# Kernel tuning notes

Hardware: AMD Instinct MI355X
Metric: run time of the kernel (lower is better)

## Reference

```python
import jax, jax.numpy as jnp
import numpy as np

E = 768      # embed_dim
P = 16       # patch size
H = 12       # heads
Dh = E // H  # 64
L = 12       # layers
IMG = 224
C = 3
N = (IMG // P) ** 2 + 1  # 197 tokens (cls + patches)
B = 64
EPS = 1e-5


def setup_inputs() -> dict:
    key = jax.random.key(0)
    ks = jax.random.split(key, 16)
    rn = lambda k, shape, s=0.02: jax.random.normal(k, shape, jnp.float32) * s
    return {
        "x": jax.random.normal(ks[0], (B, C, IMG, IMG), jnp.float32),
        "conv_w": rn(ks[1], (E, C, P, P)),
        "conv_b": jnp.zeros((E,), jnp.float32),
        "cls_embed": rn(ks[2], (1, 1, E), 1.0) * 0.02,
        "pos_embed": rn(ks[3], (1, N, E), 1.0) * 0.02,
        "ln1_s": jnp.ones((L, E), jnp.float32),
        "ln1_b": jnp.zeros((L, E), jnp.float32),
        "qkv_w": rn(ks[4], (L, H, E, 3 * Dh)),   # per-head qkv Linear weight (in,out)
        "qkv_b": jnp.zeros((L, H, 3 * Dh), jnp.float32),
        "proj_w": rn(ks[5], (L, E, E)),
        "proj_b": jnp.zeros((L, E), jnp.float32),
        "ln2_s": jnp.ones((L, E), jnp.float32),
        "ln2_b": jnp.zeros((L, E), jnp.float32),
        "fc1_w": rn(ks[6], (L, E, 4 * E)),
        "fc1_b": jnp.zeros((L, 4 * E), jnp.float32),
        "fc2_w": rn(ks[7], (L, 4 * E, E)),
        "fc2_b": jnp.zeros((L, E), jnp.float32),
    }


def _layernorm(x, s, b):
    m = jnp.mean(x, -1, keepdims=True)
    v = jnp.mean((x - m) ** 2, -1, keepdims=True)
    return (x - m) * jax.lax.rsqrt(v + EPS) * s + b


def _vit_forward(x, conv_w, conv_b, cls_embed, pos_embed,
                 ln1_s, ln1_b, qkv_w, qkv_b, proj_w, proj_b,
                 ln2_s, ln2_b, fc1_w, fc1_b, fc2_w, fc2_b):
    # Patch embedding: Conv2d stride=patch, then b c h w -> b (h w) c
    h = jax.lax.conv_general_dilated(
        x, conv_w, (P, P), 'VALID',
        dimension_numbers=('NCHW', 'OIHW', 'NCHW')) + conv_b[None, :, None, None]
    Bx = h.shape[0]
    h = h.reshape(Bx, E, -1).transpose(0, 2, 1)  # [B, 196, E]
    h = jnp.concatenate([jnp.broadcast_to(cls_embed, (Bx, 1, E)), h], axis=1)
    h = h + pos_embed  # [B, N, E]

    def block(h, p):
        l1s, l1b, qw, qb, pw, pb, l2s, l2b, f1w, f1b, f2w, f2b = p
        y = _layernorm(h, l1s, l1b)
        # per-head qkv projection, all heads at once: [B,N,H,3*Dh]
        qkv = jnp.einsum('bne,hek->bnhk', y, qw) + qb
        # torch does x.view(B,N,emb//3,3) then unbind(-1): interleaved split
        qkv = qkv.reshape(Bx, N, H, Dh, 3)
        Q, K, V = qkv[..., 0], qkv[..., 1], qkv[..., 2]
        wei = jnp.einsum('bnhd,bmhd->bhnm', Q, K) / jnp.sqrt(jnp.float32(Dh))
        wei = jax.nn.softmax(wei, axis=-1)
        att = jnp.einsum('bhnm,bmhd->bnhd', wei, V).reshape(Bx, N, H * Dh)
        h = h + att @ pw + pb  # MSA proj_back + residual (dropout=eval identity)
        y2 = _layernorm(h, l2s, l2b)
        y2 = jax.nn.gelu(y2 @ f1w + f1b, approximate=False) @ f2w + f2b
        return h + y2, None

    h, _ = jax.lax.scan(block, h, (ln1_s, ln1_b, qkv_w, qkv_b, proj_w, proj_b,
                                   ln2_s, ln2_b, fc1_w, fc1_b, fc2_w, fc2_b))
    return h


def reference(x, conv_w, conv_b, cls_embed, pos_embed,
              ln1_s, ln1_b, qkv_w, qkv_b, proj_w, proj_b,
              ln2_s, ln2_b, fc1_w, fc1_b, fc2_w, fc2_b):
    return _vit_forward(x, conv_w, conv_b, cls_embed, pos_embed,
                        ln1_s, ln1_b, qkv_w, qkv_b, proj_w, proj_b,
                        ln2_s, ln2_b, fc1_w, fc1_b, fc2_w, fc2_b)
```

## Files before the change

kernel.cpp:

```cpp
#include <hip/hip_runtime.h>
#include <hip/hip_bf16.h>
#include <math.h>

typedef __hip_bfloat16 bf16;
typedef __bf16 bf16t;
typedef __attribute__((ext_vector_type(8))) __bf16 bf16x8;
typedef __attribute__((ext_vector_type(4))) __bf16 bf16x4;
typedef __attribute__((ext_vector_type(16))) float f32x16;

#define E_DIM 768
#define HEADS 12
#define DHEAD 64
#define LAYERS 12
#define NTOK 197
#define BATCH 64
#define EPSV 1e-5f

__global__ __launch_bounds__(256) void im2col_k(const float* __restrict__ x,
                                                float* __restrict__ P,
                                                int b0, int M) {
    int task = blockIdx.x * 256 + threadIdx.x;
    if (task >= M * 96) return;
    int m = task / 96;
    int kg = task - m * 96;
    int k0 = kg * 8;
    int c = k0 >> 8, py = (k0 >> 4) & 15, px = k0 & 15;
    int bl = m / 196, pidx = m - bl * 196;
    int ph = pidx / 14, pw = pidx - ph * 14;
    const float* src = x + ((size_t)((b0 + bl) * 3 + c) * 224 + (ph * 16 + py)) * 224
                         + pw * 16 + px;
    const float4* s4 = reinterpret_cast<const float4*>(src);
    float4* d4 = reinterpret_cast<float4*>(P + (size_t)m * 768 + k0);
    d4[0] = s4[0];
    d4[1] = s4[1];
}

__global__ void embed_cls(const float* __restrict__ cls, const float* __restrict__ pos,
                          float* __restrict__ h) {
    int b = blockIdx.x, e = threadIdx.x;
    h[(size_t)b * NTOK * 768 + e] = cls[e] + pos[e];
}

__global__ __launch_bounds__(256) void layernorm_k(
    const float* __restrict__ h, float* __restrict__ y,
    const float* __restrict__ s, const float* __restrict__ bsh) {
    int tok = blockIdx.x, t = threadIdx.x;
    const float* row = h + (size_t)tok * 768;
    float v0 = row[t], v1 = row[t + 256], v2 = row[t + 512];
    float s1 = v0 + v1 + v2;
    float s2 = v0 * v0 + v1 * v1 + v2 * v2;
#pragma unroll
    for (int off = 32; off; off >>= 1) {
        s1 += __shfl_xor(s1, off);
        s2 += __shfl_xor(s2, off);
    }
    __shared__ float r1[4], r2[4];
    int wv = t >> 6, ln = t & 63;
    if (ln == 0) { r1[wv] = s1; r2[wv] = s2; }
    __syncthreads();
    s1 = r1[0] + r1[1] + r1[2] + r1[3];
    s2 = r2[0] + r2[1] + r2[2] + r2[3];
    float mean = s1 * (1.f / 768.f);
    float var = s2 * (1.f / 768.f) - mean * mean;
    float rs = rsqrtf(var + EPSV);
    float* yr = y + (size_t)tok * 768;
    yr[t]       = (v0 - mean) * rs * s[t]       + bsh[t];
    yr[t + 256] = (v1 - mean) * rs * s[t + 256] + bsh[t + 256];
    yr[t + 512] = (v2 - mean) * rs * s[t + 512] + bsh[t + 512];
}

__device__ __forceinline__ f32x16 mfma_bf16(bf16x8 a, bf16x8 b, f32x16 c) {
    return __builtin_amdgcn_mfma_f32_32x32x16_bf16(a, b, c, 0, 0, 0);
}
__device__ __forceinline__ f32x16 zero16() {
    f32x16 z;
#pragma unroll
    for (int i = 0; i < 16; ++i) z[i] = 0.f;
    return z;
}
__device__ __forceinline__ bf16x8 zbf8() {
    bf16x8 v;
#pragma unroll
    for (int i = 0; i < 8; ++i) v[i] = (__bf16)0.f;
    return v;
}
__device__ __forceinline__ unsigned pkbf(float a, float b) {
    unsigned short ua = __builtin_bit_cast(unsigned short, (__bf16)a);
    unsigned short ub = __builtin_bit_cast(unsigned short, (__bf16)b);
    return (unsigned)ua | ((unsigned)ub << 16);
}
__device__ __forceinline__ void split8(float4 u0, float4 u1, bf16x8& hi, bf16x8& lo) {
    float f[8] = {u0.x, u0.y, u0.z, u0.w, u1.x, u1.y, u1.z, u1.w};
#pragma unroll
    for (int j = 0; j < 8; ++j) {
        __bf16 h = (__bf16)f[j];
        hi[j] = h;
        lo[j] = (__bf16)(f[j] - (float)h);
    }
}

#define PLANE 2064

template <typename AT, typename CT, int TERMS>
__global__ __launch_bounds__(256, 2) void gemm_mfma(
    const AT* __restrict__ A, int lda,
    const float* __restrict__ W, int ldw,
    const float* __restrict__ bias,
    const float* __restrict__ resid,
    CT* __restrict__ C, int ldc,
    int M, int K, int flags) {
    constexpr bool SPLIT_A = (TERMS >= 3);
    const int gelu = flags & 1, perHead = flags & 2, wTrans = flags & 4;
    const int embedOut = flags & 8, qkvOut = flags & 16;
    const int n0 = blockIdx.x * 128, m0 = blockIdx.y * 128;
    const int t = threadIdx.x;

    size_t QKT = 0;
    if (qkvOut) QKT = (size_t)(M / 197) * 12 * 197 * 64;

    __shared__ __align__(16) char smem[SPLIT_A ? 4 * 8256 : 3 * 8256];
    char* sAh = smem;
    char* sWh = smem + 8256;
    char* sWl = smem + 16512;
    char* sAl = SPLIT_A ? smem + 24768 : smem;

    const AT* aptr[2]; int aoff[2]; bool aok[2];
    const float* wptr[2]; int woff[2];
    const size_t wstep = perHead ? 192 : (size_t)ldw;
#pragma unroll
    for (int p = 0; p < 2; ++p) {
        int q = t + p * 256;
        int rn = q & 127, kg = q >> 7;
        int gm = m0 + rn;
        aok[p] = gm < M;
        aptr[p] = A + (size_t)(aok[p] ? gm : 0) * lda + kg * 8;
        aoff[p] = kg * PLANE + rn * 16;
        woff[p] = kg * PLANE + rn * 16;
        if (wTrans) {
            wptr[p] = W + (size_t)(n0 + rn) * ldw + kg * 8;
        } else if (perHead) {
            int gn = n0 + rn;
            int hh = gn / 192;
            wptr[p] = W + (size_t)hh * K * 192 + (gn - hh * 192) + (size_t)(kg * 8) * 192;
        } else {
            wptr[p] = W + (n0 + rn) + (size_t)(kg * 8) * ldw;
        }
    }

    const int lane = t & 63, wv = t >> 6;
    const int wm = wv >> 1, wn = wv & 1;
    const int lr = lane & 31, lk = lane >> 5;
    const int arow0 = (wm * 64 + lr) * 16;
    const int brow0 = (wn * 64 + lr) * 16;
    f32x16 acc00 = zero16(), acc01 = zero16(), acc10 = zero16(), acc11 = zero16();

    const int nIt = K >> 5;
    for (int it = 0; it < nIt; ++it) {
        const int k0 = it << 5;
        __syncthreads();
#pragma unroll
        for (int p = 0; p < 2; ++p) {
            if constexpr (sizeof(AT) == 4) {
                float4 u0 = make_float4(0.f, 0.f, 0.f, 0.f), u1 = u0;
                if (aok[p]) {
                    const float4* s4 = reinterpret_cast<const float4*>(aptr[p] + k0);
                    u0 = s4[0]; u1 = s4[1];
                }
                bf16x8 hi, lo;
                split8(u0, u1, hi, lo);
                *reinterpret_cast<bf16x8*>(sAh + aoff[p]) = hi;
                if constexpr (SPLIT_A) *reinterpret_cast<bf16x8*>(sAl + aoff[p]) = lo;
            } else {
                bf16x8 hi = zbf8();
                if (aok[p]) hi = *reinterpret_cast<const bf16x8*>(aptr[p] + k0);
                *reinterpret_cast<bf16x8*>(sAh + aoff[p]) = hi;
            }
        }
#pragma unroll
        for (int p = 0; p < 2; ++p) {
            bf16x8 hi, lo;
            if (wTrans) {
                const float4* s4 = reinterpret_cast<const float4*>(wptr[p] + k0);
                split8(s4[0], s4[1], hi, lo);
            } else {
                const float* s = wptr[p] + (size_t)k0 * wstep;
                float4 u0, u1;
                u0.x = s[0];         u0.y = s[wstep];     u0.z = s[2 * wstep]; u0.w = s[3 * wstep];
                u1.x = s[4 * wstep]; u1.y = s[5 * wstep]; u1.z = s[6 * wstep]; u1.w = s[7 * wstep];
                split8(u0, u1, hi, lo);
            }
            *reinterpret_cast<bf16x8*>(sWh + woff[p]) = hi;
            *reinterpret_cast<bf16x8*>(sWl + woff[p]) = lo;
        }
        __syncthreads();
#pragma unroll
        for (int ks = 0; ks < 2; ++ks) {
            const int kg = ks * 2 + lk;
            const char* pa  = sAh + kg * PLANE;
            const char* pb  = sWh + kg * PLANE;
            const char* pbl = sWl + kg * PLANE;
            bf16x8 ah0 = *reinterpret_cast<const bf16x8*>(pa + arow0);
            bf16x8 ah1 = *reinterpret_cast<const bf16x8*>(pa + arow0 + 512);
            bf16x8 bh0 = *reinterpret_cast<const bf16x8*>(pb + brow0);
            bf16x8 bh1 = *reinterpret_cast<const bf16x8*>(pb + brow0 + 512);
            bf16x8 bl0 = *reinterpret_cast<const bf16x8*>(pbl + brow0);
            bf16x8 bl1 = *reinterpret_cast<const bf16x8*>(pbl + brow0 + 512);
            acc00 = mfma_bf16(ah0, bh0, acc00);
            acc01 = mfma_bf16(ah0, bh1, acc01);
            acc10 = mfma_bf16(ah1, bh0, acc10);
            acc11 = mfma_bf16(ah1, bh1, acc11);
            acc00 = mfma_bf16(ah0, bl0, acc00);
            acc01 = mfma_bf16(ah0, bl1, acc01);
            acc10 = mfma_bf16(ah1, bl0, acc10);
            acc11 = mfma_bf16(ah1, bl1, acc11);
            if constexpr (SPLIT_A) {
                const char* pal = sAl + kg * PLANE;
                bf16x8 al0 = *reinterpret_cast<const bf16x8*>(pal + arow0);
                bf16x8 al1 = *reinterpret_cast<const bf16x8*>(pal + arow0 + 512);
                acc00 = mfma_bf16(al0, bh0, acc00);
                acc01 = mfma_bf16(al0, bh1, acc01);
                acc10 = mfma_bf16(al1, bh0, acc10);
                acc11 = mfma_bf16(al1, bh1, acc11);
            }
        }
    }

    const int gcol0 = n0 + wn * 64 + lr;
#define EPILOG(ACC, MF, NF)                                                         \
    {                                                                               \
        int gcol = gcol0 + (NF) * 32;                                               \
        float bv = bias[gcol];                                                      \
        int hh2 = gcol / 192;                                                       \
        int k2 = gcol - 192 * hh2;                                                  \
        int d2 = k2 / 3;                                                            \
        int r2 = k2 - 3 * d2;                                                       \
        _Pragma("unroll")                                                           \
        for (int r = 0; r < 16; ++r) {                                              \
            int grow = m0 + wm * 64 + (MF) * 32 + (r & 3) + 8 * (r >> 2) + 4 * lk;  \
            if (grow < M) {                                                         \
                float val = ACC[r] + bv;                                            \
                if (gelu) val = 0.5f * val * (1.f + erff(val * 0.70710678f));       \
                if (qkvOut) {                                                       \
                    int b2 = grow / 197, n2 = grow - 197 * b2;                      \
                    int bh2 = b2 * 12 + hh2;                                        \
                    if (r2 == 2)                                                    \
                        C[2 * QKT + ((size_t)bh2 * 64 + d2) * 208 + n2] = (CT)val;  \
                    else                                                            \
                        C[(r2 ? QKT : 0) + ((size_t)bh2 * 197 + n2) * 64 + d2] = (CT)val; \
                } else if (embedOut) {                                              \
                    int bl2 = grow / 196;                                           \
                    int pidx = grow - bl2 * 196;                                    \
                    val += resid[(size_t)(pidx + 1) * 768 + gcol];                  \
                    C[((size_t)bl2 * 197 + pidx + 1) * ldc + gcol] = (CT)val;       \
                } else {                                                            \
                    if (resid) val += resid[(size_t)grow * ldc + gcol];             \
                    C[(size_t)grow * ldc + gcol] = (CT)val;                         \
                }                                                                   \
            }                                                                       \
        }                                                                           \
    }
    EPILOG(acc00, 0, 0)
    EPILOG(acc01, 0, 1)
    EPILOG(acc10, 1, 0)
    EPILOG(acc11, 1, 1)
#undef EPILOG
}

#define AKOFF 0
#define AVOFF 28672
#define AOOFF 61440
#define AOSTR 152
#define AOWAVE 4864

__global__ __launch_bounds__(256) void attn_mfma(
    const bf16t* __restrict__ Qb, const bf16t* __restrict__ Kb,
    const bf16t* __restrict__ Vg, bf16t* __restrict__ att) {
    __shared__ __align__(16) char lds[80896];
    const int bh = blockIdx.x;
    const int b = bh / 12, h = bh - b * 12;
    const int t = threadIdx.x;
    const int lane = t & 63, wv = t >> 6;
    const int lr = lane & 31, lk = lane >> 5;
    const int xorv = (lr & 7) << 4;

    {
        const bf16t* kb = Kb + (size_t)bh * 197 * 64;
#pragma unroll
        for (int c = 0; c < 7; ++c) {
            int idx = c * 256 + t;
            int row = idx >> 3, d8 = idx & 7;
            bf16x8 v = zbf8();
            if (row < 197) v = *(const bf16x8*)(kb + (size_t)row * 64 + d8 * 8);
            *(bf16x8*)(lds + AKOFF + row * 128 + ((d8 * 16) ^ ((row & 7) << 4))) = v;
        }
    }
    {
        const bf16t* vb = Vg + (size_t)bh * 64 * 208;
#pragma unroll
        for (int c = 0; c < 8; ++c) {
            int idx = c * 256 + t;
            int dv = idx >> 5, cc = idx & 31;
            bf16x8 v = zbf8();
            if (cc < 25) {
                v = *(const bf16x8*)(vb + (size_t)dv * 208 + cc * 8);
                if (cc == 24) { v[5] = (__bf16)0.f; v[6] = (__bf16)0.f; v[7] = (__bf16)0.f; }
            }
            *(bf16x8*)(lds + AVOFF + dv * 512 + ((cc * 16) ^ ((dv & 7) << 4))) = v;
        }
    }
    __syncthreads();

    const bf16t* qb = Qb + (size_t)bh * 197 * 64;
    char* olds = lds + AOOFF + wv * AOWAVE;

    for (int tt = wv; tt < 7; tt += 4) {
        const int i0 = tt * 32;
        int qrow = i0 + lr; if (qrow > 196) qrow = 196;
        bf16x8 qf[4];
#pragma unroll
        for (int s = 0; s < 4; ++s)
            qf[s] = *(const bf16x8*)(qb + (size_t)qrow * 64 + s * 16 + lk * 8);

        f32x16 acc[7];
#pragma unroll
        for (int kt = 0; kt < 7; ++kt) acc[kt] = zero16();
#pragma unroll
        for (int kt = 0; kt < 7; ++kt) {
#pragma unroll
            for (int s = 0; s < 4; ++s) {
                bf16x8 aK = *(const bf16x8*)(lds + AKOFF + (kt * 32 + lr) * 128
                                             + (((s * 16 + lk * 8) * 2) ^ xorv));
                acc[kt] = mfma_bf16(aK, qf[s], acc[kt]);
            }
        }
        float mx = -1e30f;
#pragma unroll
        for (int kt = 0; kt < 7; ++kt)
#pragma unroll
            for (int r = 0; r < 16; ++r) {
                int kk = kt * 32 + (r & 3) + 8 * (r >> 2) + 4 * lk;
                if (kk >= 197) acc[kt][r] = -1e30f;
                mx = fmaxf(mx, acc[kt][r]);
            }
        mx = fmaxf(mx, __shfl_xor(mx, 32));
        float sum = 0.f;
#pragma unroll
        for (int kt = 0; kt < 7; ++kt)
#pragma unroll
            for (int r = 0; r < 16; ++r) {
                float e = __expf((acc[kt][r] - mx) * 0.125f);
                acc[kt][r] = e;
                sum += e;
            }
        sum += __shfl_xor(sum, 32);
        float inv = 1.f / sum;

        f32x16 accO0 = zero16(), accO1 = zero16();
#pragma unroll
        for (int s = 0; s < 14; ++s) {
            const int kt = s >> 1, bb = (s & 1) * 8;
            unsigned A0 = pkbf(acc[kt][bb + 0], acc[kt][bb + 1]);
            unsigned A1 = pkbf(acc[kt][bb + 2], acc[kt][bb + 3]);
            unsigned C0 = pkbf(acc[kt][bb + 4], acc[kt][bb + 5]);
            unsigned C1 = pkbf(acc[kt][bb + 6], acc[kt][bb + 7]);
            unsigned x = lk ? A0 : C0, y = lk ? A1 : C1;
            unsigned rx = __shfl_xor(x, 32), ry = __shfl_xor(y, 32);
            union { unsigned u[4]; bf16x8 v; } fr;
            fr.u[0] = lk ? rx : A0; fr.u[1] = lk ? ry : A1;
            fr.u[2] = lk ? C0 : rx; fr.u[3] = lk ? C1 : ry;
            const int voff = ((s * 16 + lk * 8) * 2) ^ xorv;
            bf16x8 aV0 = *(const bf16x8*)(lds + AVOFF + lr * 512 + voff);
            bf16x8 aV1 = *(const bf16x8*)(lds + AVOFF + (lr + 32) * 512 + voff);
            accO0 = mfma_bf16(aV0, fr.v, accO0);
            accO1 = mfma_bf16(aV1, fr.v, accO1);
        }
#pragma unroll
        for (int r = 0; r < 16; r += 2) {
            int dvb = (r & 3) + 8 * (r >> 2) + 4 * lk;
            unsigned u0 = pkbf(accO0[r] * inv, accO0[r + 1] * inv);
            unsigned u1 = pkbf(accO1[r] * inv, accO1[r + 1] * inv);
            *(unsigned*)(olds + lr * AOSTR + dvb * 2) = u0;
            *(unsigned*)(olds + lr * AOSTR + (dvb + 32) * 2) = u1;
        }
        asm volatile("s_waitcnt lgkmcnt(0)" ::: "memory");
#pragma unroll
        for (int c = 0; c < 8; ++c) {
            int cid = c * 64 + lane;
            int q = cid >> 4, dc = cid & 15;
            bf16x4 v = *(const bf16x4*)(olds + q * AOSTR + dc * 8);
            int gq = i0 + q;
            if (gq < 197)
                *(bf16x4*)(att + ((size_t)b * 197 + gq) * 768 + h * 64 + dc * 4) = v;
        }
    }
}

extern "C" void kernel_launch(void* const* d_in, const int* in_sizes, int n_in,
                              void* d_out, int out_size, void* d_ws, size_t ws_size,
                              hipStream_t stream) {
    const float* x      = (const float*)d_in[0];
    const float* conv_w = (const float*)d_in[1];
    const float* conv_b = (const float*)d_in[2];
    const float* cls_e  = (const float*)d_in[3];
    const float* pos_e  = (const float*)d_in[4];
    const float* ln1_s  = (const float*)d_in[5];
    const float* ln1_b  = (const float*)d_in[6];
    const float* qkv_w  = (const float*)d_in[7];
    const float* qkv_b  = (const float*)d_in[8];
    const float* proj_w = (const float*)d_in[9];
    const float* proj_b = (const float*)d_in[10];
    const float* ln2_s  = (const float*)d_in[11];
    const float* ln2_b  = (const float*)d_in[12];
    const float* fc1_w  = (const float*)d_in[13];
    const float* fc1_b  = (const float*)d_in[14];
    const float* fc2_w  = (const float*)d_in[15];
    const float* fc2_b  = (const float*)d_in[16];

    int imgs = BATCH;
    while (imgs > 1 && (size_t)imgs * NTOK * 13824ull > ws_size) imgs >>= 1;
    size_t Mr = (size_t)imgs * NTOK;

    float* h   = (float*)d_ws;
    float* y   = h + Mr * 768;
    bf16*  att = (bf16*)(y + Mr * 768);
    bf16*  big = att + Mr * 768;

    int Mi = (int)Mr;
    int gy = (Mi + 127) / 128;
    size_t QKTOT = (size_t)imgs * 12 * 197 * 64;

    for (int b0 = 0; b0 < BATCH; b0 += imgs) {
        int Me = imgs * 196;
        im2col_k<<<dim3((Me * 96 + 255) / 256), 256, 0, stream>>>(x, y, b0, Me);
        gemm_mfma<float, float, 3><<<dim3(6, (Me + 127) / 128), 256, 0, stream>>>(
            y, 768, conv_w, 768, conv_b, pos_e, h, 768, Me, 768,  12);
        embed_cls<<<dim3(imgs), dim3(768), 0, stream>>>(cls_e, pos_e, h);

        for (int l = 0; l < LAYERS; ++l) {
            const float* qw  = qkv_w  + (long)l * HEADS * 768 * 192;
            const float* qb  = qkv_b  + (long)l * HEADS * 192;
            const float* pw  = proj_w + (long)l * 768 * 768;
            const float* pb  = proj_b + (long)l * 768;
            const float* f1w = fc1_w  + (long)l * 768 * 3072;
            const float* f1b = fc1_b  + (long)l * 3072;
            const float* f2w = fc2_w  + (long)l * 3072 * 768;
            const float* f2b = fc2_b  + (long)l * 768;

            layernorm_k<<<Mi, 256, 0, stream>>>(h, y, ln1_s + l * 768, ln1_b + l * 768);
            gemm_mfma<float, bf16t, 3><<<dim3(18, gy), 256, 0, stream>>>(
                y, 768, qw, 192, qb, nullptr, (bf16t*)big, 2304, Mi, 768,  18);
            attn_mfma<<<dim3(imgs * 12), 256, 0, stream>>>(
                (const bf16t*)big, (const bf16t*)big + QKTOT,
                (const bf16t*)big + 2 * QKTOT, (bf16t*)att);
            gemm_mfma<bf16t, float, 2><<<dim3(6, gy), 256, 0, stream>>>(
                (const bf16t*)att, 768, pw, 768, pb, h, h, 768, Mi, 768, 0);
            layernorm_k<<<Mi, 256, 0, stream>>>(h, y, ln2_s + l * 768, ln2_b + l * 768);
            gemm_mfma<float, bf16t, 3><<<dim3(24, gy), 256, 0, stream>>>(
                y, 768, f1w, 3072, f1b, nullptr, (bf16t*)big, 3072, Mi, 768,  1);
            float* outC = (l == LAYERS - 1)
                        ? (float*)d_out + (size_t)b0 * NTOK * 768 : h;
            const float* outR = h;
            gemm_mfma<bf16t, float, 2><<<dim3(6, gy), 256, 0, stream>>>(
                (const bf16t*)big, 3072, f2w, 768, f2b, outR, outC, 768, Mi, 3072, 0);
        }
    }
}
```

Before: 11.81 ms.

## Pre-split weights to transposed bf16 hi/lo and use direct global-to-LDS loads

Weights are converted once per call into transposed bf16 hi/lo planes by a tiled transpose-split kernel, and LayerNorm and im2col now emit bf16 hi/lo activations directly. The GEMM inner loop drops its per-tile fp32 loads, strided weight gathers and in-register splitting, and instead issues global_load_lds 16-byte copies straight into shared memory. This removes repeated conversion work and uncoalesced weight reads across all row blocks, at the cost of extra workspace and a few preprocessing kernels. The ragged-M edge is handled by clamping rows to M-1, and the A-row load pattern changes.

```diff
diff --git a/kernel.cpp b/kernel.cpp
--- a/kernel.cpp
+++ b/kernel.cpp
@@ -16,8 +16,60 @@
 #define BATCH 64
 #define EPSV 1e-5f
 
+__device__ __forceinline__ void split8(float4 u0, float4 u1, bf16x8& hi, bf16x8& lo) {
+    float f[8] = {u0.x, u0.y, u0.z, u0.w, u1.x, u1.y, u1.z, u1.w};
+#pragma unroll
+    for (int j = 0; j < 8; ++j) {
+        __bf16 h = (__bf16)f[j];
+        hi[j] = h;
+        lo[j] = (__bf16)(f[j] - (float)h);
+    }
+}
+
+__global__ __launch_bounds__(256) void esplit_k(const float* __restrict__ in,
+                                                bf16t* __restrict__ oh,
+                                                bf16t* __restrict__ ol, int n) {
+    int i = blockIdx.x * 256 + threadIdx.x;
+    if (i < n) {
+        float v = in[i];
+        __bf16 h = (__bf16)v;
+        oh[i] = h;
+        ol[i] = (__bf16)(v - (float)h);
+    }
+}
+
+__global__ __launch_bounds__(256) void tsplit_k(
+    const float* __restrict__ in, long inStride,
+    bf16t* __restrict__ oh, bf16t* __restrict__ ol, long outStride,
+    int K, int N) {
+    int z = blockIdx.z;
+    in += (long)z * inStride;
+    oh += (long)z * outStride;
+    ol += (long)z * outStride;
+    __shared__ float tile[32][33];
+    int k0 = blockIdx.x * 32, n0 = blockIdx.y * 32;
+    int tx = threadIdx.x & 31, ty = threadIdx.x >> 5;
+#pragma unroll
+    for (int i = 0; i < 4; ++i) {
+        int k = k0 + ty + 8 * i, n = n0 + tx;
+        tile[ty + 8 * i][tx] = (k < K && n < N) ? in[(long)k * N + n] : 0.f;
+    }
+    __syncthreads();
+#pragma unroll
+    for (int i = 0; i < 4; ++i) {
+        int n = n0 + ty + 8 * i, k = k0 + tx;
+        if (n < N && k < K) {
+            float v = tile[tx][ty + 8 * i];
+            __bf16 h = (__bf16)v;
+            oh[(long)n * K + k] = h;
+            ol[(long)n * K + k] = (__bf16)(v - (float)h);
+        }
+    }
+}
+
 __global__ __launch_bounds__(256) void im2col_k(const float* __restrict__ x,
-                                                float* __restrict__ P,
+                                                bf16t* __restrict__ Ph,
+                                                bf16t* __restrict__ Pl,
                                                 int b0, int M) {
     int task = blockIdx.x * 256 + threadIdx.x;
     if (task >= M * 96) return;
@@ -30,9 +82,10 @@
     const float* src = x + ((size_t)((b0 + bl) * 3 + c) * 224 + (ph * 16 + py)) * 224
                          + pw * 16 + px;
     const float4* s4 = reinterpret_cast<const float4*>(src);
-    float4* d4 = reinterpret_cast<float4*>(P + (size_t)m * 768 + k0);
-    d4[0] = s4[0];
-    d4[1] = s4[1];
+    bf16x8 hi, lo;
+    split8(s4[0], s4[1], hi, lo);
+    *reinterpret_cast<bf16x8*>(Ph + (size_t)m * 768 + k0) = hi;
+    *reinterpret_cast<bf16x8*>(Pl + (size_t)m * 768 + k0) = lo;
 }
 
 __global__ void embed_cls(const float* __restrict__ cls, const float* __restrict__ pos,
@@ -42,7 +95,7 @@
 }
 
 __global__ __launch_bounds__(256) void layernorm_k(
-    const float* __restrict__ h, float* __restrict__ y,
+    const float* __restrict__ h, bf16t* __restrict__ yh, bf16t* __restrict__ yl,
     const float* __restrict__ s, const float* __restrict__ bsh) {
     int tok = blockIdx.x, t = threadIdx.x;
     const float* row = h + (size_t)tok * 768;
@@ -63,10 +116,16 @@
     float mean = s1 * (1.f / 768.f);
     float var = s2 * (1.f / 768.f) - mean * mean;
     float rs = rsqrtf(var + EPSV);
-    float* yr = y + (size_t)tok * 768;
-    yr[t]       = (v0 - mean) * rs * s[t]       + bsh[t];
-    yr[t + 256] = (v1 - mean) * rs * s[t + 256] + bsh[t + 256];
-    yr[t + 512] = (v2 - mean) * rs * s[t + 512] + bsh[t + 512];
+    size_t base = (size_t)tok * 768;
+#pragma unroll
+    for (int c = 0; c < 3; ++c) {
+        int idx = t + c * 256;
+        float v = (c == 0) ? v0 : (c == 1) ? v1 : v2;
+        float o = (v - mean) * rs * s[idx] + bsh[idx];
+        __bf16 hh = (__bf16)o;
+        yh[base + idx] = hh;
+        yl[base + idx] = (__bf16)(o - (float)hh);
+    }
 }
 
 __device__ __forceinline__ f32x16 mfma_bf16(bf16x8 a, bf16x8 b, f32x16 c) {
@@ -89,29 +148,24 @@
     unsigned short ub = __builtin_bit_cast(unsigned short, (__bf16)b);
     return (unsigned)ua | ((unsigned)ub << 16);
 }
-__device__ __forceinline__ void split8(float4 u0, float4 u1, bf16x8& hi, bf16x8& lo) {
-    float f[8] = {u0.x, u0.y, u0.z, u0.w, u1.x, u1.y, u1.z, u1.w};
-#pragma unroll
-    for (int j = 0; j < 8; ++j) {
-        __bf16 h = (__bf16)f[j];
-        hi[j] = h;
-        lo[j] = (__bf16)(f[j] - (float)h);
-    }
+__device__ __forceinline__ void gld16(const bf16t* g, char* l) {
+    __builtin_amdgcn_global_load_lds(
+        (const __attribute__((address_space(1))) unsigned int*)g,
+        (__attribute__((address_space(3))) unsigned int*)l, 16, 0, 0);
 }
 
 #define PLANE 2064
 
-template <typename AT, typename CT, int TERMS>
+template <typename CT, int TERMS>
 __global__ __launch_bounds__(256, 2) void gemm_mfma(
-    const AT* __restrict__ A, int lda,
-    const float* __restrict__ W, int ldw,
+    const bf16t* __restrict__ Ah, const bf16t* __restrict__ Al, int lda,
+    const bf16t* __restrict__ Wh, const bf16t* __restrict__ Wl,
     const float* __restrict__ bias,
     const float* __restrict__ resid,
     CT* __restrict__ C, int ldc,
     int M, int K, int flags) {
     constexpr bool SPLIT_A = (TERMS >= 3);
-    const int gelu = flags & 1, perHead = flags & 2, wTrans = flags & 4;
-    const int embedOut = flags & 8, qkvOut = flags & 16;
+    const int gelu = flags & 1, embedOut = flags & 8, qkvOut = flags & 16;
     const int n0 = blockIdx.x * 128, m0 = blockIdx.y * 128;
     const int t = threadIdx.x;
 
@@ -124,73 +178,38 @@
     char* sWl = smem + 16512;
     char* sAl = SPLIT_A ? smem + 24768 : smem;
 
-    const AT* aptr[2]; int aoff[2]; bool aok[2];
-    const float* wptr[2]; int woff[2];
-    const size_t wstep = perHead ? 192 : (size_t)ldw;
-#pragma unroll
-    for (int p = 0; p < 2; ++p) {
-        int q = t + p * 256;
-        int rn = q & 127, kg = q >> 7;
-        int gm = m0 + rn;
-        aok[p] = gm < M;
-        aptr[p] = A + (size_t)(aok[p] ? gm : 0) * lda + kg * 8;
-        aoff[p] = kg * PLANE + rn * 16;
-        woff[p] = kg * PLANE + rn * 16;
-        if (wTrans) {
-            wptr[p] = W + (size_t)(n0 + rn) * ldw + kg * 8;
-        } else if (perHead) {
-            int gn = n0 + rn;
-            int hh = gn / 192;
-            wptr[p] = W + (size_t)hh * K * 192 + (gn - hh * 192) + (size_t)(kg * 8) * 192;
-        } else {
-            wptr[p] = W + (n0 + rn) + (size_t)(kg * 8) * ldw;
-        }
-    }
-
     const int lane = t & 63, wv = t >> 6;
     const int wm = wv >> 1, wn = wv & 1;
     const int lr = lane & 31, lk = lane >> 5;
+
+    const int kgA = wv >> 1;
+    const int row0 = (wv & 1) * 64;
+    int arow = m0 + row0 + lane; if (arow >= M) arow = M - 1;
+    const int wrow = n0 + row0 + lane;
+    const bf16t* aS  = Ah + (size_t)arow * lda + kgA * 8;
+    const bf16t* alS = SPLIT_A ? Al + (size_t)arow * lda + kgA * 8 : aS;
+    const bf16t* wS  = Wh + (size_t)wrow * K + kgA * 8;
+    const bf16t* wlS = Wl + (size_t)wrow * K + kgA * 8;
+    char* dA  = sAh + kgA * PLANE + row0 * 16;
+    char* dAl = sAl + kgA * PLANE + row0 * 16;
+    char* dW  = sWh + kgA * PLANE + row0 * 16;
+    char* dWl = sWl + kgA * PLANE + row0 * 16;
+
     const int arow0 = (wm * 64 + lr) * 16;
     const int brow0 = (wn * 64 + lr) * 16;
     f32x16 acc00 = zero16(), acc01 = zero16(), acc10 = zero16(), acc11 = zero16();
 
-    const int nIt = K >> 5;
-    for (int it = 0; it < nIt; ++it) {
-        const int k0 = it << 5;
+    for (int k0 = 0; k0 < K; k0 += 32) {
         __syncthreads();
-#pragma unroll
-        for (int p = 0; p < 2; ++p) {
-            if constexpr (sizeof(AT) == 4) {
-                float4 u0 = make_float4(0.f, 0.f, 0.f, 0.f), u1 = u0;
-                if (aok[p]) {
-                    const float4* s4 = reinterpret_cast<const float4*>(aptr[p] + k0);
-                    u0 = s4[0]; u1 = s4[1];
-                }
-                bf16x8 hi, lo;
-                split8(u0, u1, hi, lo);
-                *reinterpret_cast<bf16x8*>(sAh + aoff[p]) = hi;
-                if constexpr (SPLIT_A) *reinterpret_cast<bf16x8*>(sAl + aoff[p]) = lo;
-            } else {
-                bf16x8 hi = zbf8();
-                if (aok[p]) hi = *reinterpret_cast<const bf16x8*>(aptr[p] + k0);
-                *reinterpret_cast<bf16x8*>(sAh + aoff[p]) = hi;
-            }
-        }
-#pragma unroll
-        for (int p = 0; p < 2; ++p) {
-            bf16x8 hi, lo;
-            if (wTrans) {
-                const float4* s4 = reinterpret_cast<const float4*>(wptr[p] + k0);
-                split8(s4[0], s4[1], hi, lo);
-            } else {
-                const float* s = wptr[p] + (size_t)k0 * wstep;
-                float4 u0, u1;
-                u0.x = s[0];         u0.y = s[wstep];     u0.z = s[2 * wstep]; u0.w = s[3 * wstep];
-                u1.x = s[4 * wstep]; u1.y = s[5 * wstep]; u1.z = s[6 * wstep]; u1.w = s[7 * wstep];
-                split8(u0, u1, hi, lo);
-            }
-            *reinterpret_cast<bf16x8*>(sWh + woff[p]) = hi;
-            *reinterpret_cast<bf16x8*>(sWl + woff[p]) = lo;
+        gld16(aS + k0,       dA);
+        gld16(aS + k0 + 16,  dA + 2 * PLANE);
+        gld16(wS + k0,       dW);
+        gld16(wS + k0 + 16,  dW + 2 * PLANE);
+        gld16(wlS + k0,      dWl);
+        gld16(wlS + k0 + 16, dWl + 2 * PLANE);
+        if constexpr (SPLIT_A) {
+            gld16(alS + k0,      dAl);
+            gld16(alS + k0 + 16, dAl + 2 * PLANE);
         }
         __syncthreads();
 #pragma unroll
@@ -416,14 +435,54 @@
     const float* fc2_w  = (const float*)d_in[15];
     const float* fc2_b  = (const float*)d_in[16];
 
+    const size_t QKV_E = 2304ull * 768, PRJ_E = 768ull * 768;
+    const size_t FC1_E = 3072ull * 768, FC2_E = 3072ull * 768;
+    const size_t perLayerE = QKV_E + PRJ_E + FC1_E + FC2_E;
+    const size_t convE = 768ull * 768;
+    const size_t wAllB = 12ull * perLayerE * 2 * 2;
+    const size_t wOneB = perLayerE * 2 * 2;
+    const size_t convB = convE * 2 * 2;
+
     int imgs = BATCH;
-    while (imgs > 1 && (size_t)imgs * NTOK * 13824ull > ws_size) imgs >>= 1;
+    bool preAll = false;
+    for (;;) {
+        size_t act = (size_t)imgs * NTOK * 13824ull;
+        if (act + convB + wAllB <= ws_size) { preAll = true; break; }
+        if (act + convB + wOneB <= ws_size) { preAll = false; break; }
+        if (imgs == 1) break;
+        imgs >>= 1;
+    }
     size_t Mr = (size_t)imgs * NTOK;
 
-    float* h   = (float*)d_ws;
-    float* y   = h + Mr * 768;
-    bf16*  att = (bf16*)(y + Mr * 768);
-    bf16*  big = att + Mr * 768;
+    float* h    = (float*)d_ws;
+    bf16t* yhi  = (bf16t*)(h + Mr * 768);
+    bf16t* ylo  = yhi + Mr * 768;
+    bf16t* att  = ylo + Mr * 768;
+    bf16t* big  = att + Mr * 768;
+    bf16t* cvH  = big + Mr * 3072;
+    bf16t* cvL  = cvH + convE;
+    bf16t* wb   = cvL + convE;
+
+    bf16t *Qh, *Ql, *Ph, *Pl, *F1h, *F1l, *F2h, *F2l;
+    if (preAll) {
+        Qh = wb;            Ql = Qh + 12 * QKV_E;
+        Ph = Ql + 12 * QKV_E; Pl = Ph + 12 * PRJ_E;
+        F1h = Pl + 12 * PRJ_E; F1l = F1h + 12 * FC1_E;
+        F2h = F1l + 12 * FC1_E; F2l = F2h + 12 * FC2_E;
+    } else {
+        Qh = wb;            Ql = Qh + QKV_E;
+        Ph = Ql + QKV_E;    Pl = Ph + PRJ_E;
+        F1h = Pl + PRJ_E;   F1l = F1h + FC1_E;
+        F2h = F1l + FC1_E;  F2l = F2h + FC2_E;
+    }
+
+    esplit_k<<<(int)((convE + 255) / 256), 256, 0, stream>>>(conv_w, cvH, cvL, (int)convE);
+    if (preAll) {
+        tsplit_k<<<dim3(24, 6, 144), 256, 0, stream>>>(qkv_w, 768l * 192, Qh, Ql, 192l * 768, 768, 192);
+        tsplit_k<<<dim3(24, 24, 12), 256, 0, stream>>>(proj_w, (long)PRJ_E, Ph, Pl, (long)PRJ_E, 768, 768);
+        tsplit_k<<<dim3(24, 96, 12), 256, 0, stream>>>(fc1_w, (long)FC1_E, F1h, F1l, (long)FC1_E, 768, 3072);
+        tsplit_k<<<dim3(96, 24, 12), 256, 0, stream>>>(fc2_w, (long)FC2_E, F2h, F2l, (long)FC2_E, 3072, 768);
+    }
 
     int Mi = (int)Mr;
     int gy = (Mi + 127) / 128;
@@ -431,37 +490,49 @@
 
     for (int b0 = 0; b0 < BATCH; b0 += imgs) {
         int Me = imgs * 196;
-        im2col_k<<<dim3((Me * 96 + 255) / 256), 256, 0, stream>>>(x, y, b0, Me);
-        gemm_mfma<float, float, 3><<<dim3(6, (Me + 127) / 128), 256, 0, stream>>>(
-            y, 768, conv_w, 768, conv_b, pos_e, h, 768, Me, 768,  12);
+        im2col_k<<<dim3((Me * 96 + 255) / 256), 256, 0, stream>>>(x, yhi, ylo, b0, Me);
+        gemm_mfma<float, 3><<<dim3(6, (Me + 127) / 128), 256, 0, stream>>>(
+            yhi, ylo, 768, cvH, cvL, conv_b, pos_e, h, 768, Me, 768,  8);
         embed_cls<<<dim3(imgs), dim3(768), 0, stream>>>(cls_e, pos_e, h);
 
         for (int l = 0; l < LAYERS; ++l) {
-            const float* qw  = qkv_w  + (long)l * HEADS * 768 * 192;
-            const float* qb  = qkv_b  + (long)l * HEADS * 192;
-            const float* pw  = proj_w + (long)l * 768 * 768;
-            const float* pb  = proj_b + (long)l * 768;
-            const float* f1w = fc1_w  + (long)l * 768 * 3072;
-            const float* f1b = fc1_b  + (long)l * 3072;
-            const float* f2w = fc2_w  + (long)l * 3072 * 768;
-            const float* f2b = fc2_b  + (long)l * 768;
-
-            layernorm_k<<<Mi, 256, 0, stream>>>(h, y, ln1_s + l * 768, ln1_b + l * 768);
-            gemm_mfma<float, bf16t, 3><<<dim3(18, gy), 256, 0, stream>>>(
-                y, 768, qw, 192, qb, nullptr, (bf16t*)big, 2304, Mi, 768,  18);
+            const bf16t *qh, *ql, *ph, *pl, *f1h, *f1l, *f2h, *f2l;
+            if (preAll) {
+                qh = Qh + (size_t)l * QKV_E;  ql = Ql + (size_t)l * QKV_E;
+                ph = Ph + (size_t)l * PRJ_E;  pl = Pl + (size_t)l * PRJ_E;
+                f1h = F1h + (size_t)l * FC1_E; f1l = F1l + (size_t)l * FC1_E;
+                f2h = F2h + (size_t)l * FC2_E; f2l = F2l + (size_t)l * FC2_E;
+            } else {
+                tsplit_k<<<dim3(24, 6, 12), 256, 0, stream>>>(
+                    qkv_w + (size_t)l * 12 * QKV_E / 12 * 1, 768l * 192, Qh, Ql, 192l * 768, 768, 192);
+                tsplit_k<<<dim3(24, 24, 1), 256, 0, stream>>>(
+                    proj_w + (size_t)l * PRJ_E, 0, Ph, Pl, 0, 768, 768);
+                tsplit_k<<<dim3(24, 96, 1), 256, 0, stream>>>(
+                    fc1_w + (size_t)l * FC1_E, 0, F1h, F1l, 0, 768, 3072);
+                tsplit_k<<<dim3(96, 24, 1), 256, 0, stream>>>(
+                    fc2_w + (size_t)l * FC2_E, 0, F2h, F2l, 0, 3072, 768);
+                qh = Qh; ql = Ql; ph = Ph; pl = Pl;
+                f1h = F1h; f1l = F1l; f2h = F2h; f2l = F2l;
+            }
+            const float* qb  = qkv_b  + (size_t)l * HEADS * 192;
+            const float* pb  = proj_b + (size_t)l * 768;
+            const float* f1b = fc1_b  + (size_t)l * 3072;
+            const float* f2b = fc2_b  + (size_t)l * 768;
+
+            layernorm_k<<<Mi, 256, 0, stream>>>(h, yhi, ylo, ln1_s + l * 768, ln1_b + l * 768);
+            gemm_mfma<bf16t, 3><<<dim3(18, gy), 256, 0, stream>>>(
+                yhi, ylo, 768, qh, ql, qb, nullptr, big, 2304, Mi, 768,  16);
             attn_mfma<<<dim3(imgs * 12), 256, 0, stream>>>(
-                (const bf16t*)big, (const bf16t*)big + QKTOT,
-                (const bf16t*)big + 2 * QKTOT, (bf16t*)att);
-            gemm_mfma<bf16t, float, 2><<<dim3(6, gy), 256, 0, stream>>>(
-                (const bf16t*)att, 768, pw, 768, pb, h, h, 768, Mi, 768, 0);
-            layernorm_k<<<Mi, 256, 0, stream>>>(h, y, ln2_s + l * 768, ln2_b + l * 768);
-            gemm_mfma<float, bf16t, 3><<<dim3(24, gy), 256, 0, stream>>>(
-                y, 768, f1w, 3072, f1b, nullptr, (bf16t*)big, 3072, Mi, 768,  1);
+                big, big + QKTOT, big + 2 * QKTOT, att);
+            gemm_mfma<float, 2><<<dim3(6, gy), 256, 0, stream>>>(
+                att, nullptr, 768, ph, pl, pb, h, h, 768, Mi, 768, 0);
+            layernorm_k<<<Mi, 256, 0, stream>>>(h, yhi, ylo, ln2_s + l * 768, ln2_b + l * 768);
+            gemm_mfma<bf16t, 3><<<dim3(24, gy), 256, 0, stream>>>(
+                yhi, ylo, 768, f1h, f1l, f1b, nullptr, big, 3072, Mi, 768,  1);
             float* outC = (l == LAYERS - 1)
                         ? (float*)d_out + (size_t)b0 * NTOK * 768 : h;
-            const float* outR = h;
-            gemm_mfma<bf16t, float, 2><<<dim3(6, gy), 256, 0, stream>>>(
-                (const bf16t*)big, 3072, f2w, 768, f2b, outR, outC, 768, Mi, 3072, 0);
-        }
-    }
-}
+            gemm_mfma<float, 2><<<dim3(6, gy), 256, 0, stream>>>(
+                big, nullptr, 3072, f2h, f2l, f2b, h, outC, 768, Mi, 3072, 0);
+        }
+    }
+}
```

Result: slower. 13.10 ms (+11.0%).
